# Kernel tuning notes

Measured on AMD Instinct MI355X. Metric: run time of the kernel, lower is better.

## Reference

```python
import jax, jax.numpy as jnp
import numpy as np

BITS = 4            # bits per quantized weight
NPACK = 8           # 32-bit container / 4-bit values
CBITS = 32          # compression dtype bit width (int32)
GROUP = 128         # quantization group size along in_features
IN = 4096
OUT = 11008
BATCH = 32


def _dequant(packed_weight, scale):
    # Unpack signed int4 values: (p << (32 - 4*(e+1))) >> 28, arithmetic shift
    # sign-extends, matching the torch recover() path for weight_dtype=int8.
    e = jnp.arange(NPACK, dtype=jnp.int32)                      # [8]
    shifted = (packed_weight[:, :, None] << (CBITS - BITS * (e + 1))) >> (CBITS - BITS)  # [O, I/8, 8]
    w_int = shifted.reshape(OUT, IN).astype(jnp.int8)           # signed int4 in int8
    # Per-group scale: reshape to [O*I/GROUP, GROUP] * [O*I/GROUP, 1]
    w = w_int.astype(jnp.float32).reshape(-1, GROUP) * scale.reshape(-1, 1)
    return w.reshape(OUT, IN)


def setup_inputs() -> dict:
    key = jax.random.key(0)
    k1, k2, k3, k4 = jax.random.split(key, 4)
    x = jax.random.normal(k1, (BATCH, IN), dtype=jnp.float32)
    packed_weight = jax.random.randint(
        k2, (OUT, IN // NPACK), jnp.iinfo(jnp.int32).min, jnp.iinfo(jnp.int32).max,
        dtype=jnp.int32)
    scale = jax.random.uniform(k3, (OUT, IN // GROUP), dtype=jnp.float32,
                               minval=0.001, maxval=0.02)
    bias = jax.random.normal(k4, (OUT,), dtype=jnp.float32)
    return {"x": x, "packed_weight": packed_weight, "scale": scale, "bias": bias}


def reference(x, packed_weight, scale, bias):
    W = _dequant(packed_weight, scale)      # [OUT, IN] fp32
    return x @ W.T + bias                    # F.linear(x, W, bias)
```

## Files before the change

### kernel.cpp

```cpp
#include <hip/hip_runtime.h>
#include <hip/hip_bf16.h>

#define IN_F   4096
#define OUT_F  11008
#define BATCH  32
#define NG     32
#define PACKS  512

typedef __bf16 bf16x8_t __attribute__((ext_vector_type(8)));
typedef float  floatx4_t __attribute__((ext_vector_type(4)));

__global__ __launch_bounds__(256) void prep_x(const float* __restrict__ x,
                                              unsigned short* __restrict__ xp) {
  int c  = blockIdx.x * 256 + threadIdx.x;
  int mm = c & 31;
  int k0 = ((c >> 5) & 3) * 32 + ((c >> 7) & 3) * 8 + (c >> 9) * 128;
  const float* src = x + mm * IN_F + k0;
  float4 f0 = *(const float4*)(src);
  float4 f1 = *(const float4*)(src + 4);
  float v[8] = {f0.x, f0.y, f0.z, f0.w, f1.x, f1.y, f1.z, f1.w};
  union { unsigned short s[8]; uint4 u; } r;
#pragma unroll
  for (int j = 0; j < 8; ++j) {
    unsigned int u = __float_as_uint(v[j]);
    unsigned int rnd = ((u >> 16) & 1u) + 0x7fffu;
    r.s[j] = (unsigned short)((u + rnd) >> 16);
  }
  *(uint4*)(xp + c * 8) = r.u;
}

__device__ inline bf16x8_t unpack8(int p) {
  union { unsigned short u[8]; bf16x8_t v; } r;
#pragma unroll
  for (int j = 0; j < 8; ++j) {
    int nib = (p << (28 - 4 * j)) >> 28;
    float f = (float)nib;
    r.u[j] = (unsigned short)(__float_as_uint(f) >> 16);
  }
  return r.v;
}

__device__ inline bf16x8_t load_frag(const unsigned short* p) {
  union { uint4 u; bf16x8_t v; } x;
  x.u = *(const uint4*)p;
  return x.v;
}

__global__ __launch_bounds__(256) void wql_main(
    const int* __restrict__ pw, const float* __restrict__ scale,
    const float* __restrict__ bias, const unsigned short* __restrict__ xp,
    float* __restrict__ out) {
  __shared__ float lds[4][BATCH * 32];

  const int tid = threadIdx.x;
  const int l   = tid & 63;
  const int w   = tid >> 6;
  const int col = l & 15;
  const int q   = l >> 4;
  const int n0  = blockIdx.x * 32;
  const int nA  = n0 + col;
  const int nB  = n0 + 16 + col;

  floatx4_t acc00 = {0.f, 0.f, 0.f, 0.f};
  floatx4_t acc01 = {0.f, 0.f, 0.f, 0.f};
  floatx4_t acc10 = {0.f, 0.f, 0.f, 0.f};
  floatx4_t acc11 = {0.f, 0.f, 0.f, 0.f};

  const int g0 = w * 8;
#pragma unroll 1
  for (int gi = 0; gi < 8; ++gi) {
    const int gg = g0 + gi;
    int4 pA = *(const int4*)(pw + nA * PACKS + gg * 16 + q * 4);
    int4 pB = *(const int4*)(pw + nB * PACKS + gg * 16 + q * 4);
    float sA = scale[nA * NG + gg];
    float sB = scale[nB * NG + gg];

    const unsigned short* ab = xp + (gg * 512 + q * 32 + col) * 8;
    bf16x8_t a0[4], a1[4];
#pragma unroll
    for (int t = 0; t < 4; ++t) {
      a0[t] = load_frag(ab + t * 1024);
      a1[t] = load_frag(ab + t * 1024 + 128);
    }

    floatx4_t t00 = {0.f, 0.f, 0.f, 0.f};
    floatx4_t t01 = {0.f, 0.f, 0.f, 0.f};
    floatx4_t t10 = {0.f, 0.f, 0.f, 0.f};
    floatx4_t t11 = {0.f, 0.f, 0.f, 0.f};
    int pAv[4] = {pA.x, pA.y, pA.z, pA.w};
    int pBv[4] = {pB.x, pB.y, pB.z, pB.w};
#pragma unroll
    for (int t = 0; t < 4; ++t) {
      bf16x8_t b0 = unpack8(pAv[t]);
      bf16x8_t b1 = unpack8(pBv[t]);
      t00 = __builtin_amdgcn_mfma_f32_16x16x32_bf16(a0[t], b0, t00, 0, 0, 0);
      t10 = __builtin_amdgcn_mfma_f32_16x16x32_bf16(a1[t], b0, t10, 0, 0, 0);
      t01 = __builtin_amdgcn_mfma_f32_16x16x32_bf16(a0[t], b1, t01, 0, 0, 0);
      t11 = __builtin_amdgcn_mfma_f32_16x16x32_bf16(a1[t], b1, t11, 0, 0, 0);
    }
#pragma unroll
    for (int r = 0; r < 4; ++r) {
      acc00[r] += t00[r] * sA;
      acc10[r] += t10[r] * sA;
      acc01[r] += t01[r] * sB;
      acc11[r] += t11[r] * sB;
    }
  }

#pragma unroll
  for (int r = 0; r < 4; ++r) {
    int row = q * 4 + r;
    lds[w][row * 32 + col]             = acc00[r];
    lds[w][row * 32 + 16 + col]        = acc01[r];
    lds[w][(16 + row) * 32 + col]      = acc10[r];
    lds[w][(16 + row) * 32 + 16 + col] = acc11[r];
  }
  __syncthreads();

  for (int e = tid; e < BATCH * 32; e += 256) {
    int row = e >> 5, cl = e & 31;
    float s = lds[0][e] + lds[1][e] + lds[2][e] + lds[3][e];
    out[row * OUT_F + n0 + cl] = s + bias[n0 + cl];
  }
}

extern "C" void kernel_launch(void* const* d_in, const int* in_sizes, int n_in,
                              void* d_out, int out_size, void* d_ws, size_t ws_size,
                              hipStream_t stream) {
  const float* x     = (const float*)d_in[0];
  const int*   pw    = (const int*)d_in[1];
  const float* scale = (const float*)d_in[2];
  const float* bias  = (const float*)d_in[3];
  float* out = (float*)d_out;
  unsigned short* xp = (unsigned short*)d_ws;

  hipLaunchKernelGGL(prep_x, dim3(16384 / 256), dim3(256), 0, stream, x, xp);
  hipLaunchKernelGGL(wql_main, dim3(OUT_F / 32), dim3(256), 0, stream,
                     pw, scale, bias, xp, out);
}
```

Measured before the change: 86.20 us.

## Split K across 8 waves and software-prefetch next group's weights

The main kernel now runs 512 threads per block, with each of 8 waves covering 4 quantization groups instead of 4 waves covering 8, so more waves are in flight to hide memory latency. The packed weights and scales for the next group are loaded before the current group is computed, overlapping global loads with unpacking and MFMA work. The x-prep kernel switches to 64-thread blocks. The cost is a larger LDS reduction buffer, an 8-way final sum, and more register pressure from the prefetched values.

```diff
diff --git a/kernel.cpp b/kernel.cpp
--- a/kernel.cpp
+++ b/kernel.cpp
@@ -10,9 +10,9 @@
 typedef __bf16 bf16x8_t __attribute__((ext_vector_type(8)));
 typedef float  floatx4_t __attribute__((ext_vector_type(4)));
 
-__global__ __launch_bounds__(256) void prep_x(const float* __restrict__ x,
-                                              unsigned short* __restrict__ xp) {
-  int c  = blockIdx.x * 256 + threadIdx.x;
+__global__ __launch_bounds__(64) void prep_x(const float* __restrict__ x,
+                                             unsigned short* __restrict__ xp) {
+  int c  = blockIdx.x * 64 + threadIdx.x;
   int mm = c & 31;
   int k0 = ((c >> 5) & 3) * 32 + ((c >> 7) & 3) * 8 + (c >> 9) * 128;
   const float* src = x + mm * IN_F + k0;
@@ -46,11 +46,11 @@
   return x.v;
 }
 
-__global__ __launch_bounds__(256) void wql_main(
+__global__ __launch_bounds__(512, 4) void wql_main(
     const int* __restrict__ pw, const float* __restrict__ scale,
     const float* __restrict__ bias, const unsigned short* __restrict__ xp,
     float* __restrict__ out) {
-  __shared__ float lds[4][BATCH * 32];
+  __shared__ float lds[8][BATCH * 32];
 
   const int tid = threadIdx.x;
   const int l   = tid & 63;
@@ -66,14 +66,26 @@
   floatx4_t acc10 = {0.f, 0.f, 0.f, 0.f};
   floatx4_t acc11 = {0.f, 0.f, 0.f, 0.f};
 
-  const int g0 = w * 8;
+  const int g0 = w * 4;
+  const int* pwA = pw + nA * PACKS + g0 * 16 + q * 4;
+  const int* pwB = pw + nB * PACKS + g0 * 16 + q * 4;
+
+  int4 pA = *(const int4*)pwA;
+  int4 pB = *(const int4*)pwB;
+  float sA = scale[nA * NG + g0];
+  float sB = scale[nB * NG + g0];
+
 #pragma unroll 1
-  for (int gi = 0; gi < 8; ++gi) {
+  for (int gi = 0; gi < 4; ++gi) {
     const int gg = g0 + gi;
-    int4 pA = *(const int4*)(pw + nA * PACKS + gg * 16 + q * 4);
-    int4 pB = *(const int4*)(pw + nB * PACKS + gg * 16 + q * 4);
-    float sA = scale[nA * NG + gg];
-    float sB = scale[nB * NG + gg];
+    int4 cA = pA, cB = pB;
+    float csA = sA, csB = sB;
+    if (gi < 3) {
+      pA = *(const int4*)(pwA + (gi + 1) * 16);
+      pB = *(const int4*)(pwB + (gi + 1) * 16);
+      sA = scale[nA * NG + gg + 1];
+      sB = scale[nB * NG + gg + 1];
+    }
 
     const unsigned short* ab = xp + (gg * 512 + q * 32 + col) * 8;
     bf16x8_t a0[4], a1[4];
@@ -87,8 +99,8 @@
     floatx4_t t01 = {0.f, 0.f, 0.f, 0.f};
     floatx4_t t10 = {0.f, 0.f, 0.f, 0.f};
     floatx4_t t11 = {0.f, 0.f, 0.f, 0.f};
-    int pAv[4] = {pA.x, pA.y, pA.z, pA.w};
-    int pBv[4] = {pB.x, pB.y, pB.z, pB.w};
+    int pAv[4] = {cA.x, cA.y, cA.z, cA.w};
+    int pBv[4] = {cB.x, cB.y, cB.z, cB.w};
 #pragma unroll
     for (int t = 0; t < 4; ++t) {
       bf16x8_t b0 = unpack8(pAv[t]);
@@ -100,10 +112,10 @@
     }
 #pragma unroll
     for (int r = 0; r < 4; ++r) {
-      acc00[r] += t00[r] * sA;
-      acc10[r] += t10[r] * sA;
-      acc01[r] += t01[r] * sB;
-      acc11[r] += t11[r] * sB;
+      acc00[r] += t00[r] * csA;
+      acc10[r] += t10[r] * csA;
+      acc01[r] += t01[r] * csB;
+      acc11[r] += t11[r] * csB;
     }
   }
 
@@ -117,9 +129,10 @@
   }
   __syncthreads();
 
-  for (int e = tid; e < BATCH * 32; e += 256) {
+  for (int e = tid; e < BATCH * 32; e += 512) {
     int row = e >> 5, cl = e & 31;
-    float s = lds[0][e] + lds[1][e] + lds[2][e] + lds[3][e];
+    float s = lds[0][e] + lds[1][e] + lds[2][e] + lds[3][e]
+            + lds[4][e] + lds[5][e] + lds[6][e] + lds[7][e];
     out[row * OUT_F + n0 + cl] = s + bias[n0 + cl];
   }
 }
@@ -134,7 +147,7 @@
   float* out = (float*)d_out;
   unsigned short* xp = (unsigned short*)d_ws;
 
-  hipLaunchKernelGGL(prep_x, dim3(16384 / 256), dim3(256), 0, stream, x, xp);
-  hipLaunchKernelGGL(wql_main, dim3(OUT_F / 32), dim3(256), 0, stream,
+  hipLaunchKernelGGL(prep_x, dim3(16384 / 64), dim3(64), 0, stream, x, xp);
+  hipLaunchKernelGGL(wql_main, dim3(OUT_F / 32), dim3(512), 0, stream,
                      pw, scale, bias, xp, out);
 }
```

Result: slower. 88.60 us (+2.8%).
